# Optimization experiments

Measured on AMD Instinct MI355X. Metric: run time of the kernel, lower is better.

The kernel has to match this reference:

```python
import jax, jax.numpy as jnp
import numpy as np

B_SZ = 8
G = 2048
D_MODEL = 512
D_STATE = 128
D_CONV = 4
EXPAND = 2
HEADDIM = 64
D_INNER = EXPAND * D_MODEL          # 1024
NHEADS = D_INNER // HEADDIM         # 16
CONV_DIM = D_INNER + 2 * D_STATE    # 1280
D_IN_PROJ = 2 * D_INNER + 2 * D_STATE + NHEADS  # 2320
ID_DIM = 128
CHR_DIM = 64
N_CHR = 25
F_LOCUS = 32
PATH_DIM = 128
GENE_FEAT = ID_DIM + PATH_DIM + 2 * CHR_DIM  # 384
N_PERT = 10000
P_DIM = 128


def silu(x):
    return x * jax.nn.sigmoid(x)


def causal_dw_conv(x, w, b):
    # x: (B,L,C), w: (C,K), b: (C,)  causal depthwise conv (left pad K-1)
    K = w.shape[1]
    L = x.shape[1]
    xp = jnp.pad(x, ((0, 0), (K - 1, 0), (0, 0)))
    out = b[None, None, :]
    for k in range(K):
        out = out + xp[:, k:k + L, :] * w[:, k][None, None, :]
    return out


def mamba2(u, in_w, conv_w, conv_b, dt_bias, A_log, Dp, norm_w, out_w):
    # u: (B,L,d_model) -> (B,L,d_model); mamba_ssm Mamba2 defaults, ngroups=1
    Bb, L, _ = u.shape
    zxbcdt = u @ in_w.T                                   # (B,L,D_IN_PROJ)
    z = zxbcdt[..., :D_INNER]
    xBC = zxbcdt[..., D_INNER:D_INNER + CONV_DIM]
    dt = zxbcdt[..., D_INNER + CONV_DIM:]                 # (B,L,H)
    xBC = silu(causal_dw_conv(xBC, conv_w, conv_b))
    x = xBC[..., :D_INNER].reshape(Bb, L, NHEADS, HEADDIM)
    Bm = xBC[..., D_INNER:D_INNER + D_STATE]              # (B,L,N)
    Cm = xBC[..., D_INNER + D_STATE:]                     # (B,L,N)
    dt = jax.nn.softplus(dt + dt_bias)                    # (B,L,H)
    dA = jnp.exp(dt * (-jnp.exp(A_log)))                  # (B,L,H)

    def step(h, inp):
        dA_t, dt_t, B_t, C_t, x_t = inp
        h = dA_t[:, :, None, None] * h + jnp.einsum('bh,bn,bhp->bhpn', dt_t, B_t, x_t)
        y = jnp.einsum('bhpn,bn->bhp', h, C_t)
        return h, y

    h0 = jnp.zeros((Bb, NHEADS, HEADDIM, D_STATE), u.dtype)
    xs = (dA.transpose(1, 0, 2), dt.transpose(1, 0, 2),
          Bm.transpose(1, 0, 2), Cm.transpose(1, 0, 2), x.transpose(1, 0, 2, 3))
    _, ys = jax.lax.scan(step, h0, xs)                    # ys: (L,B,H,P)
    y = ys.transpose(1, 0, 2, 3) + Dp[None, None, :, None] * x
    y = y.reshape(Bb, L, D_INNER)
    # gated RMSNorm (norm_before_gate=False): norm(y * silu(z))
    y = y * silu(z)
    y = y * jax.lax.rsqrt(jnp.mean(y * y, axis=-1, keepdims=True) + 1e-5) * norm_w
    return y @ out_w.T


def setup_inputs() -> dict:
    key = jax.random.key(0)
    ks = iter(jax.random.split(key, 48))

    def nrm(shape, scale):
        return jax.random.normal(next(ks), shape, jnp.float32) * scale

    inp = {}
    inp['perturbation_idx'] = jax.random.randint(next(ks), (B_SZ,), 0, N_PERT)
    inp['chr_idx'] = jax.random.randint(next(ks), (G,), 0, N_CHR)
    inp['locus_fourier'] = nrm((G, 2 * F_LOCUS), 1.0)
    inp['pathway_features'] = nrm((G, PATH_DIM), 1.0)
    inp['pert_emb'] = nrm((N_PERT, P_DIM), 0.02)
    inp['gene_id_emb'] = nrm((G, ID_DIM), 0.02)
    inp['chr_emb'] = nrm((N_CHR, CHR_DIM), 0.02)
    inp['locus_w'] = nrm((CHR_DIM, 2 * F_LOCUS), (2 * F_LOCUS) ** -0.5)
    inp['locus_b'] = jnp.zeros((CHR_DIM,), jnp.float32)
    inp['cond_w'] = nrm((GENE_FEAT, P_DIM), P_DIM ** -0.5)
    inp['cond_b'] = jnp.zeros((GENE_FEAT,), jnp.float32)
    inp['in_w'] = nrm((D_MODEL, GENE_FEAT), GENE_FEAT ** -0.5)
    inp['in_b'] = jnp.zeros((D_MODEL,), jnp.float32)
    inp['head_w'] = nrm((1, D_MODEL), D_MODEL ** -0.5)
    inp['head_b'] = jnp.zeros((1,), jnp.float32)
    for p in ('f_', 'b_'):
        inp[p + 'in_w'] = nrm((D_IN_PROJ, D_MODEL), D_MODEL ** -0.5)
        inp[p + 'conv_w'] = nrm((CONV_DIM, D_CONV), D_CONV ** -0.5)
        inp[p + 'conv_b'] = jnp.zeros((CONV_DIM,), jnp.float32)
        inp[p + 'dt_bias'] = nrm((NHEADS,), 0.5)
        inp[p + 'A_log'] = jnp.log(jax.random.uniform(next(ks), (NHEADS,), jnp.float32, 1.0, 16.0))
        inp[p + 'D'] = jnp.ones((NHEADS,), jnp.float32)
        inp[p + 'norm_w'] = jnp.ones((D_INNER,), jnp.float32)
        inp[p + 'out_w'] = nrm((D_MODEL, D_INNER), D_INNER ** -0.5)
    return inp


def reference(perturbation_idx, chr_idx, locus_fourier, pathway_features,
              pert_emb, gene_id_emb, chr_emb, locus_w, locus_b,
              cond_w, cond_b, in_w, in_b, head_w, head_b,
              f_in_w, f_conv_w, f_conv_b, f_dt_bias, f_A_log, f_D, f_norm_w, f_out_w,
              b_in_w, b_conv_w, b_conv_b, b_dt_bias, b_A_log, b_D, b_norm_w, b_out_w):
    B = perturbation_idx.shape[0]
    cond = pert_emb[perturbation_idx] @ cond_w.T + cond_b          # (B, GENE_FEAT)
    e_chr = chr_emb[chr_idx]                                        # (G, CHR_DIM)
    e_locus = jax.nn.gelu(locus_fourier @ locus_w.T + locus_b, approximate=False)
    gene_feat = jnp.concatenate([gene_id_emb, pathway_features, e_chr, e_locus], axis=1)  # (G, GENE_FEAT)
    seq = jnp.concatenate([cond[:, None, :],
                           jnp.broadcast_to(gene_feat[None], (B,) + gene_feat.shape)], axis=1)
    seq = seq @ in_w.T + in_b                                       # (B, G+1, d_model)
    h_fwd = mamba2(seq, f_in_w, f_conv_w, f_conv_b, f_dt_bias, f_A_log, f_D, f_norm_w, f_out_w)
    h_bwd = jnp.flip(mamba2(jnp.flip(seq, axis=1), b_in_w, b_conv_w, b_conv_b,
                            b_dt_bias, b_A_log, b_D, b_norm_w, b_out_w), axis=1)
    H = h_fwd + h_bwd
    return H[:, 1:, :] @ head_w.T + head_b                          # (B, G, 1)
```

## Files before the change

kernel.cpp:

```cpp
#include <hip/hip_runtime.h>
#include <hip/hip_bf16.h>
#include <hip/hip_fp16.h>
#include <math.h>

#define DPROJ 2320
#define CONVD 1280

typedef __attribute__((ext_vector_type(8))) short bf16x8;
typedef __attribute__((ext_vector_type(4))) float f32x4;

__device__ __forceinline__ float siluf(float x) { return x / (1.f + __expf(-x)); }
__device__ __forceinline__ float bfu(unsigned short s) { return __uint_as_float(((unsigned)s) << 16); }
__device__ __forceinline__ unsigned short f2bf(float f) {
    unsigned u = __float_as_uint(f);
    unsigned r = (u + 0x7FFFu + ((u >> 16) & 1u)) >> 16;
    return (unsigned short)r;
}
__device__ __forceinline__ unsigned short f2h(float f) {
    __half h = __float2half(f);
    return *(unsigned short*)&h;
}
__device__ __forceinline__ float h2f(unsigned short s) {
    __half h = *(__half*)&s;
    return __half2float(h);
}


__global__ void gg_kernel(const int* __restrict__ chridx, const float* __restrict__ gid,
                          const float* __restrict__ path, const float* __restrict__ chrE,
                          const int* __restrict__ pidx, const float* __restrict__ pertE,
                          float* __restrict__ gf, float* __restrict__ cemb,
                          float* __restrict__ wf2, float* __restrict__ wb2) {
    int blk = blockIdx.x, tid = threadIdx.x;
    if (blk < 3072) {
        int idx = blk * 256 + tid;
        int g = idx / 384, j = idx % 384;
        float v;
        if (j < 128)      v = gid[(size_t)g * 128 + j];
        else if (j < 256) v = path[(size_t)g * 128 + (j - 128)];
        else if (j < 320) v = chrE[(size_t)chridx[g] * 64 + (j - 256)];
        else return;
        gf[idx] = v;
    } else if (blk < 3076) {
        int idx = (blk - 3072) * 256 + tid;
        int b = idx >> 7, k = idx & 127;
        cemb[idx] = pertE[(size_t)pidx[b] * 128 + k];
    } else {
        wf2[tid * 4 + 0] = 0.f; wf2[tid * 4 + 1] = 0.f;
        wf2[tid * 4 + 2] = 0.f; wf2[tid * 4 + 3] = 0.f;
        wb2[tid * 4 + 0] = 0.f; wb2[tid * 4 + 1] = 0.f;
        wb2[tid * 4 + 2] = 0.f; wb2[tid * 4 + 3] = 0.f;
    }
}

__global__ void wfold_kernel(const float* __restrict__ headW,
                             const float* __restrict__ fOutW, const float* __restrict__ fNw,
                             const float* __restrict__ bOutW, const float* __restrict__ bNw,
                             float* __restrict__ wf2, float* __restrict__ wb2) {
    int blk = blockIdx.x;
    int dir = blk >> 6;
    int rem = blk & 63;
    int dseg = rem >> 4, mseg = rem & 15;
    int tid = threadIdx.x;
    int d = dseg * 256 + tid;
    const float* W = dir ? bOutW : fOutW;
    float s = 0.f;
#pragma unroll
    for (int m = mseg * 32; m < mseg * 32 + 32; ++m)
        s += headW[m] * W[(size_t)m * 1024 + d];
    const float* nw = dir ? bNw : fNw;
    atomicAdd(&(dir ? wb2 : wf2)[d], s * nw[d]);
}


__global__ void tobf4_kernel(const float* __restrict__ inW, const float* __restrict__ fInW,
                             const float* __restrict__ bInW, const float* __restrict__ gf,
                             unsigned short* __restrict__ inW2, unsigned short* __restrict__ fInW2,
                             unsigned short* __restrict__ bInW2, unsigned short* __restrict__ gf2) {
    size_t idx = (size_t)blockIdx.x * 256 + threadIdx.x;
    const size_t A = 512UL * 384, B5 = 2432UL * 512;
    if (idx < A) {
        inW2[idx] = f2bf(inW[idx]);
    } else if (idx < A + B5) {
        size_t k = idx - A; int m = k / 512, kk = k % 512;
        fInW2[k] = f2bf(m < 2320 ? fInW[(size_t)m * 512 + kk] : 0.f);
    } else if (idx < A + 2 * B5) {
        size_t k = idx - A - B5; int m = k / 512, kk = k % 512;
        bInW2[k] = f2bf(m < 2320 ? bInW[(size_t)m * 512 + kk] : 0.f);
    } else {
        size_t k = idx - A - 2 * B5;
        gf2[k] = f2bf(gf[k]);
    }
}

__global__ void tobf_kernel(const float* __restrict__ in, unsigned short* __restrict__ out,
                            int M, int K, int Mpad) {
    int idx = blockIdx.x * 256 + threadIdx.x;
    if (idx >= Mpad * K) return;
    int m = idx / K, k = idx % K;
    float v = (m < M) ? in[(size_t)m * K + k] : 0.f;
    out[idx] = f2bf(v);
}


__global__ __launch_bounds__(256) void mfma_gemm_kernel(
    const unsigned short* __restrict__ A2, const unsigned short* __restrict__ W2,
    const float* __restrict__ bias, float* __restrict__ C,
    int N, int K2, int ldc) {
    __shared__ __align__(16) unsigned short Al[128 * 40];
    __shared__ __align__(16) unsigned short Bl[128 * 40];
    const int tid = threadIdx.x;
    const int bm = blockIdx.y * 128, bn = blockIdx.x * 128;
    const int lane = tid & 63, wave = tid >> 6;
    const int wm = (wave >> 1) * 64, wn = (wave & 1) * 64;
    f32x4 acc[4][4];
#pragma unroll
    for (int i = 0; i < 4; ++i)
#pragma unroll
        for (int j = 0; j < 4; ++j) acc[i][j] = (f32x4){0.f, 0.f, 0.f, 0.f};

    for (int k0 = 0; k0 < K2; k0 += 32) {
        __syncthreads();
#pragma unroll
        for (int s = 0; s < 2; ++s) {
            int ch = tid + 256 * s;
            int row = ch >> 2, q = ch & 3;
            uint4 va = *(const uint4*)&A2[(size_t)(bm + row) * K2 + k0 + q * 8];
            *(uint4*)&Al[row * 40 + q * 8] = va;
            uint4 vb = *(const uint4*)&W2[(size_t)(bn + row) * K2 + k0 + q * 8];
            *(uint4*)&Bl[row * 40 + q * 8] = vb;
        }
        __syncthreads();
        bf16x8 af[4], bfr[4];
#pragma unroll
        for (int i = 0; i < 4; ++i)
            af[i] = *(const bf16x8*)&Al[(wm + i * 16 + (lane & 15)) * 40 + (lane >> 4) * 8];
#pragma unroll
        for (int j = 0; j < 4; ++j)
            bfr[j] = *(const bf16x8*)&Bl[(wn + j * 16 + (lane & 15)) * 40 + (lane >> 4) * 8];
#pragma unroll
        for (int i = 0; i < 4; ++i)
#pragma unroll
            for (int j = 0; j < 4; ++j)
                acc[i][j] = __builtin_amdgcn_mfma_f32_16x16x32_bf16(af[i], bfr[j], acc[i][j], 0, 0, 0);
    }
#pragma unroll
    for (int i = 0; i < 4; ++i) {
        int m = bm + wm + i * 16 + (lane >> 4) * 4;
#pragma unroll
        for (int j = 0; j < 4; ++j) {
            int n = bn + wn + j * 16 + (lane & 15);
            if (n < N) {
                float bv = bias ? bias[n] : 0.f;
#pragma unroll
                for (int r = 0; r < 4; ++r)
                    C[(size_t)(m + r) * ldc + n] = acc[i][j][r] + bv;
            }
        }
    }
}


__global__ __launch_bounds__(256) void gemm_kernel(
    const float* __restrict__ A, const float* __restrict__ W,
    const float* __restrict__ bias, float* __restrict__ C,
    int M, int N, int K, int ldc, int act) {
    __shared__ __align__(16) float As[16][68];
    __shared__ __align__(16) float Ws[16][68];
    const int tid = threadIdx.x;
    const int tx = tid & 15, ty = tid >> 4;
    const int bm = blockIdx.y * 64, bn = blockIdx.x * 64;
    const int lr = tid >> 2;
    const int lk = (tid & 3) * 4;
    float acc[4][4];
#pragma unroll
    for (int i = 0; i < 4; ++i)
#pragma unroll
        for (int j = 0; j < 4; ++j) acc[i][j] = 0.f;

    for (int k0 = 0; k0 < K; k0 += 16) {
        const int am = bm + lr;
        const int wn = bn + lr;
        float4 av = make_float4(0.f, 0.f, 0.f, 0.f), wv = make_float4(0.f, 0.f, 0.f, 0.f);
        if (am < M) av = *(const float4*)&A[(size_t)am * K + k0 + lk];
        if (wn < N) wv = *(const float4*)&W[(size_t)wn * K + k0 + lk];
        __syncthreads();
        As[lk + 0][lr] = av.x; As[lk + 1][lr] = av.y; As[lk + 2][lr] = av.z; As[lk + 3][lr] = av.w;
        Ws[lk + 0][lr] = wv.x; Ws[lk + 1][lr] = wv.y; Ws[lk + 2][lr] = wv.z; Ws[lk + 3][lr] = wv.w;
        __syncthreads();
#pragma unroll
        for (int kk = 0; kk < 16; ++kk) {
            float4 a = *(const float4*)&As[kk][ty * 4];
            float4 w = *(const float4*)&Ws[kk][tx * 4];
            float aa[4] = {a.x, a.y, a.z, a.w}, ww[4] = {w.x, w.y, w.z, w.w};
#pragma unroll
            for (int i = 0; i < 4; ++i)
#pragma unroll
                for (int j = 0; j < 4; ++j) acc[i][j] += aa[i] * ww[j];
        }
    }
#pragma unroll
    for (int i = 0; i < 4; ++i) {
        const int m = bm + ty * 4 + i;
        if (m >= M) continue;
#pragma unroll
        for (int j = 0; j < 4; ++j) {
            const int n = bn + tx * 4 + j;
            if (n >= N) continue;
            float v = acc[i][j] + (bias ? bias[n] : 0.f);
            if (act == 1) v = 0.5f * v * (1.f + erff(v * 0.70710678118654752f));
            C[(size_t)m * ldc + n] = v;
        }
    }
}


__global__ void elem_kernel(const float* __restrict__ zxf, const float* __restrict__ zxb,
                            const float* __restrict__ zxc,
                            const float* __restrict__ fDtB, const float* __restrict__ bDtB,
                            unsigned short* __restrict__ szF, unsigned short* __restrict__ szB,
                            float* __restrict__ dtFsT, float* __restrict__ dtBsT,
                            float* __restrict__ dtFp) {
    size_t idx = (size_t)blockIdx.x * 256 + threadIdx.x;
    const size_t SZ = 2048UL * 1024;
    if (idx < SZ) {
        size_t j = idx >> 10, d = idx & 1023;
        szF[idx] = f2h(siluf(zxf[j * DPROJ + d]));
    } else if (idx < 2 * SZ) {
        size_t k = idx - SZ;
        size_t j = k >> 10, d = k & 1023;
        szB[k] = f2h(siluf(zxb[j * DPROJ + d]));
    } else if (idx < 2 * SZ + 32768) {
        int k = (int)(idx - 2 * SZ);
        int r = k >> 4, hh = k & 15;
        float raw = zxf[(size_t)r * DPROJ + 2304 + hh] + fDtB[hh];
        dtFsT[hh * 2048 + r] = (raw > 20.f) ? raw : log1pf(expf(raw));
    } else if (idx < 2 * SZ + 65536) {
        int k = (int)(idx - 2 * SZ - 32768);
        int r = k >> 4, hh = k & 15;
        float raw = zxb[(size_t)(2047 - r) * DPROJ + 2304 + hh] + bDtB[hh];
        dtBsT[hh * 2048 + r] = (raw > 20.f) ? raw : log1pf(expf(raw));
    } else if (idx < 2 * SZ + 65536 + 128) {
        int k = (int)(idx - 2 * SZ - 65536);
        int b = k >> 4, hh = k & 15;
        float raw = zxc[(size_t)b * DPROJ + 2304 + hh] + fDtB[hh];
        dtFp[k] = (raw > 20.f) ? raw : log1pf(expf(raw));
    }
}

__global__ void cum_kernel(const float* __restrict__ dtFsT, const float* __restrict__ dtBsT,
                           const float* __restrict__ fAlog, const float* __restrict__ bAlog,
                           float* __restrict__ cumF, float* __restrict__ cumB) {
    int id = blockIdx.x * 256 + threadIdx.x;
    int dir = id >> 9, k = id & 511, h = k >> 5, c = k & 31;
    const float* dtT = dir ? dtBsT : dtFsT;
    const float* Al = dir ? bAlog : fAlog;
    float* cum = dir ? cumB : cumF;
    float a = -expf(Al[h]);
    float acc = 0.f;
    for (int s4 = 0; s4 < 16; ++s4) {
        float4 v = *(const float4*)&dtT[h * 2048 + c * 64 + s4 * 4];
        float4 o;
        acc += v.x * a; o.x = acc;
        acc += v.y * a; o.y = acc;
        acc += v.z * a; o.z = acc;
        acc += v.w * a; o.w = acc;
        *(float4*)&cum[h * 2048 + c * 64 + s4 * 4] = o;
    }
}


__global__ void convFsh_kernel(const float* __restrict__ zxf, const float* __restrict__ cw,
                               const float* __restrict__ cb,
                               unsigned short* __restrict__ bc16, unsigned short* __restrict__ x16) {
    int idx = blockIdx.x * 256 + threadIdx.x;
    if (idx >= 2045 * 1280) return;
    int t4 = idx / 1280, c = idx % 1280;
    float4 w4 = *(const float4*)&cw[c * 4];
    float acc = cb[c];
    acc += zxf[(size_t)(t4 + 0) * DPROJ + 1024 + c] * w4.x;
    acc += zxf[(size_t)(t4 + 1) * DPROJ + 1024 + c] * w4.y;
    acc += zxf[(size_t)(t4 + 2) * DPROJ + 1024 + c] * w4.z;
    acc += zxf[(size_t)(t4 + 3) * DPROJ + 1024 + c] * w4.w;
    float r = siluf(acc);
    if (c >= 1024) bc16[(size_t)t4 * 256 + (c - 1024)] = f2bf(r);
    else           x16[(size_t)t4 * 1024 + c] = f2bf(r);
}

__global__ void convFpb_kernel(const float* __restrict__ zxf, const float* __restrict__ zxc,
                               const float* __restrict__ cw, const float* __restrict__ cb,
                               float* __restrict__ outp, unsigned short* __restrict__ bc16,
                               unsigned short* __restrict__ x16) {
    int idx = blockIdx.x * 256 + threadIdx.x;
    int b = idx / 5120;
    int r = idx % 5120;
    int t = r / 1280, c = r % 1280;
    float4 w4 = *(const float4*)&cw[c * 4];
    float w[4] = {w4.x, w4.y, w4.z, w4.w};
    float acc = cb[c];
#pragma unroll
    for (int k = 0; k < 4; ++k) {
        int j = t - 3 + k;
        float x = 0.f;
        if (j == 0)      x = zxc[(size_t)b * DPROJ + 1024 + c];
        else if (j >= 1) x = zxf[(size_t)(j - 1) * DPROJ + 1024 + c];
        acc += x * w[k];
    }
    float rr = siluf(acc);
    outp[idx] = rr;
    if (c >= 1024) bc16[(size_t)(b * 4 + t) * 256 + (c - 1024)] = f2bf(rr);
    else           x16[(size_t)(b * 4 + t) * 1024 + c] = f2bf(rr);
}

__global__ void convBsh_kernel(const float* __restrict__ zxb, const float* __restrict__ cw,
                               const float* __restrict__ cb,
                               unsigned short* __restrict__ bc16, unsigned short* __restrict__ x16) {
    int idx = blockIdx.x * 256 + threadIdx.x;
    int s = idx / 1280, c = idx % 1280;
    float4 w4 = *(const float4*)&cw[c * 4];
    float w[4] = {w4.x, w4.y, w4.z, w4.w};
    float acc = cb[c];
#pragma unroll
    for (int k = 0; k < 4; ++k) {
        int j = s - 3 + k;
        if (j >= 0) acc += zxb[(size_t)(2047 - j) * DPROJ + 1024 + c] * w[k];
    }
    float r = siluf(acc);
    if (c >= 1024) bc16[(size_t)s * 256 + (c - 1024)] = f2bf(r);
    else           x16[(size_t)s * 1024 + c] = f2bf(r);
}


__global__ __launch_bounds__(256) void intra_kernel(
    const unsigned short* __restrict__ bcF, const unsigned short* __restrict__ bcFp,
    const unsigned short* __restrict__ bcB,
    const unsigned short* __restrict__ xF16, const unsigned short* __restrict__ xFp16,
    const unsigned short* __restrict__ xB16,
    const float* __restrict__ dtFsT, const float* __restrict__ dtBsT,
    const float* __restrict__ cumF, const float* __restrict__ cumB,
    unsigned short* __restrict__ YiF0, unsigned short* __restrict__ YiFs,
    unsigned short* __restrict__ YiB,
    unsigned short* __restrict__ UF0, unsigned short* __restrict__ UFs,
    unsigned short* __restrict__ UB) {
    __shared__ __align__(16) unsigned char smraw[63232];
    unsigned short* Bt = (unsigned short*)smraw;
    unsigned short* Ct = (unsigned short*)(smraw + 17408);
    unsigned short* Sm = (unsigned short*)(smraw + 17408);
    unsigned short* BT = (unsigned short*)(smraw + 34816);
    unsigned short* XT = (unsigned short*)(smraw + 53248);
    float* scum = (float*)(smraw + 62464);
// ... 132 lines not shown

    const int nm = wave * 32;
    f32x4 acc3[2][4];
#pragma unroll
    for (int i = 0; i < 2; ++i)
#pragma unroll
        for (int j = 0; j < 4; ++j) acc3[i][j] = (f32x4){0.f, 0.f, 0.f, 0.f};
#pragma unroll
    for (int ks = 0; ks < 2; ++ks) {
        float ev[8];
#pragma unroll
        for (int jj = 0; jj < 8; ++jj) ev[jj] = se[ks * 32 + quad * 8 + jj];
        bf16x8 bfx[4];
#pragma unroll
        for (int j = 0; j < 4; ++j) {
            bf16x8 xs = *(const bf16x8*)&XT[(j * 16 + l15) * 72 + ks * 32 + quad * 8];
#pragma unroll
            for (int jj = 0; jj < 8; ++jj)
                bfx[j][jj] = (short)f2bf(bfu((unsigned short)xs[jj]) * ev[jj]);
        }
        bf16x8 af[2];
#pragma unroll
        for (int i = 0; i < 2; ++i)
            af[i] = *(const bf16x8*)&BT[(nm + i * 16 + l15) * 72 + ks * 32 + quad * 8];
#pragma unroll
        for (int i = 0; i < 2; ++i)
#pragma unroll
            for (int j = 0; j < 4; ++j)
                acc3[i][j] = __builtin_amdgcn_mfma_f32_16x16x32_bf16(af[i], bfx[j], acc3[i][j], 0, 0, 0);
    }
#pragma unroll
    for (int i = 0; i < 2; ++i)
#pragma unroll
        for (int j = 0; j < 4; ++j) {
            int p = j * 16 + l15;
            int n0 = nm + i * 16 + quad * 4;
            ushort4 o = make_ushort4(f2bf(acc3[i][j][0]), f2bf(acc3[i][j][1]),
                                     f2bf(acc3[i][j][2]), f2bf(acc3[i][j][3]));
            *(ushort4*)&Uout[p * 128 + n0] = o;
        }
}


__global__ void cbm_kernel(const float* __restrict__ convFp, const unsigned short* __restrict__ bcF,
                           const float* __restrict__ dtFp, const float* __restrict__ cumF,
                           const unsigned short* __restrict__ UF0,
                           float* __restrict__ cb0, unsigned short* __restrict__ Mb) {
    int blk = blockIdx.x, tid = threadIdx.x;
    if (blk < 32) {
        int idx = blk * 256 + tid;
        int b = idx >> 10, r = idx & 1023, h = r >> 6, tl = r & 63;
        int t = tl + 1;
        const float* b0 = convFp + (size_t)(b * 4) * CONVD;
        float s = 0.f;
        if (t < 4) {
            const float* crow = convFp + (size_t)(b * 4 + t) * CONVD;
            for (int n = 0; n < 128; ++n) s += crow[1152 + n] * b0[1024 + n];
        } else {
            const unsigned short* cr = bcF + (size_t)(t - 4) * 256 + 128;
            for (int n = 0; n < 128; ++n) s += bfu(cr[n]) * b0[1024 + n];
        }
        cb0[(b * 16 + h) * 64 + tl] = s * dtFp[b * 16 + h];
    } else {
        int bh = blk - 32;
        int b = bh >> 4, h = bh & 15;
        float D0 = __expf(cumF[h * 2048 + 63]);
        float dt0 = dtFp[b * 16 + h];
        const float* row0 = convFp + (size_t)(b * 4) * CONVD;
        const unsigned short* u = UF0 + (size_t)(b * 16 + h) * 8192;
        unsigned short* m = Mb + (size_t)(b * 16 + h) * 8192;
        for (int e4 = tid; e4 < 2048; e4 += 256) {
            int e = e4 * 4, p = e >> 7, n0 = e & 127;
            float s = D0 * dt0 * row0[h * 64 + p];
            float4 B4 = *(const float4*)&row0[1024 + n0];
            ushort4 uv = *(const ushort4*)&u[e];
            ushort4 o = make_ushort4(f2bf(s * B4.x + bfu(uv.x)), f2bf(s * B4.y + bfu(uv.y)),
                                     f2bf(s * B4.z + bfu(uv.z)), f2bf(s * B4.w + bfu(uv.w)));
            *(ushort4*)&m[e] = o;
        }
    }
}


__global__ void tpsi_kernel(const unsigned short* __restrict__ UFs, const unsigned short* __restrict__ UB,
                            const float* __restrict__ cumF, const float* __restrict__ cumB,
                            unsigned short* __restrict__ Tst, float* __restrict__ psiF) {
    int blk = blockIdx.x;
    int dir = blk >> 7, h = (blk >> 3) & 15, q8 = blk & 7;
    int tid = threadIdx.x;
    const unsigned short* U = dir ? UB : UFs;
    const float* cum = dir ? cumB : cumF;
    unsigned short* T = Tst + (size_t)(dir * 16 + h) * 32 * 8192;
    if (dir == 0 && q8 == 0 && tid == 0) {
        float ps = 1.f;
        for (int c = 1; c < 32; ++c) {
            psiF[h * 32 + c] = ps;
            ps *= __expf(cumF[h * 2048 + c * 64 + 63]);
        }
    }
    const size_t e = (size_t)q8 * 1024 + 4 * tid;
    float4 st = make_float4(0.f, 0.f, 0.f, 0.f);
    const int c0 = dir ? 0 : 1;
    ushort4 u = *(const ushort4*)&U[((size_t)c0 * 16 + h) * 8192 + e];
    for (int c = c0; c < 32; ++c) {
        ushort4 un = make_ushort4(0, 0, 0, 0);
        if (c + 1 < 32) un = *(const ushort4*)&U[((size_t)(c + 1) * 16 + h) * 8192 + e];
        float Dc = __expf(cum[h * 2048 + c * 64 + 63]);
        ushort4 o = make_ushort4(f2bf(st.x), f2bf(st.y), f2bf(st.z), f2bf(st.w));
        *(ushort4*)&T[(size_t)c * 8192 + e] = o;
        st.x = Dc * st.x + bfu(u.x);
        st.y = Dc * st.y + bfu(u.y);
        st.z = Dc * st.z + bfu(u.z);
        st.w = Dc * st.w + bfu(u.w);
        u = un;
    }
}


__global__ __launch_bounds__(256) void yt_kernel(
    const unsigned short* __restrict__ bcF, const unsigned short* __restrict__ bcB,
    const unsigned short* __restrict__ Tst,
    unsigned short* __restrict__ YtF, unsigned short* __restrict__ YtB) {
    const int iid = blockIdx.x;
    int dir, h, c;
    if (iid < 496) { dir = 0; c = 1 + (iid >> 4); h = iid & 15; }
    else           { int k = iid - 496; dir = 1; c = k >> 4; h = k & 15; }
    const unsigned short* Cbase = (dir == 0)
        ? bcF + ((size_t)(64 * c - 3)) * 256 + 128
        : bcB + ((size_t)(64 * c)) * 256 + 128;
    const unsigned short* Tp = Tst + ((size_t)(dir * 16 + h) * 32 + c) * 8192;
    unsigned short* Yt = (dir == 0 ? YtF : YtB) + (size_t)(c * 16 + h) * 4096;
    const int tid = threadIdx.x;
    const int lane = tid & 63, wave = tid >> 6;
    const int quad = lane >> 4, l15 = lane & 15;
    const int pm = (wave >> 1) * 32, tb = (wave & 1) * 32;
    f32x4 acc[2][2];
#pragma unroll
    for (int i = 0; i < 2; ++i)
#pragma unroll
        for (int j = 0; j < 2; ++j) acc[i][j] = (f32x4){0.f, 0.f, 0.f, 0.f};
#pragma unroll
    for (int ks = 0; ks < 4; ++ks) {
        bf16x8 af[2], bfr[2];
#pragma unroll
        for (int i = 0; i < 2; ++i)
            af[i] = *(const bf16x8*)&Tp[(size_t)(pm + i * 16 + l15) * 128 + ks * 32 + quad * 8];
#pragma unroll
        for (int j = 0; j < 2; ++j)
            bfr[j] = *(const bf16x8*)&Cbase[(size_t)(tb + j * 16 + l15) * 256 + ks * 32 + quad * 8];
#pragma unroll
        for (int i = 0; i < 2; ++i)
#pragma unroll
            for (int j = 0; j < 2; ++j)
                acc[i][j] = __builtin_amdgcn_mfma_f32_16x16x32_bf16(af[i], bfr[j], acc[i][j], 0, 0, 0);
    }
#pragma unroll
    for (int i = 0; i < 2; ++i)
#pragma unroll
        for (int j = 0; j < 2; ++j) {
            int t = tb + j * 16 + l15;
            int p0 = pm + i * 16 + quad * 4;
            ushort4 o = make_ushort4(f2bf(acc[i][j][0]), f2bf(acc[i][j][1]),
                                     f2bf(acc[i][j][2]), f2bf(acc[i][j][3]));
            *(ushort4*)&Yt[t * 64 + p0] = o;
        }
}


__global__ __launch_bounds__(256) void gate_kernel(
    const unsigned short* __restrict__ bcF,
    const unsigned short* __restrict__ Mb, const float* __restrict__ psiF,
    const unsigned short* __restrict__ YtF, const unsigned short* __restrict__ YtB,
    const unsigned short* __restrict__ xF16, const unsigned short* __restrict__ xFp16,
    const unsigned short* __restrict__ xB16,
    const unsigned short* __restrict__ szF, const unsigned short* __restrict__ szB,
    const float* __restrict__ convFp,
    const float* __restrict__ cumF, const float* __restrict__ cumB,
    const unsigned short* __restrict__ YiF0, const unsigned short* __restrict__ YiFs,
    const unsigned short* __restrict__ YiB,
    const float* __restrict__ cb0,
    const float* __restrict__ fD, const float* __restrict__ bD,
    const float* __restrict__ wf2, const float* __restrict__ wb2,
    float* __restrict__ aF, float* __restrict__ aB) {
    __shared__ __align__(16) float Ysm[64 * 68];

    const int iid = blockIdx.x;
    int dir, b = 0, h, cg;
    if (iid < 1024) { dir = 0; b = iid >> 7; int r = iid & 127; h = r >> 3; cg = r & 7; }
    else            { int k = iid - 1024; dir = 1; h = k >> 3; cg = k & 7; }
    const int tid = threadIdx.x, tx = tid & 15, ty = tid >> 4;
    const int lane = tid & 63, wave = tid >> 6;
    const int quad = lane >> 4, l15 = lane & 15;

    const float Dh = (dir ? bD : fD)[h];
    const float* wvp = dir ? wb2 : wf2;
    float4 wreg = *(const float4*)&wvp[h * 64 + tx * 4];
    const float* cumA = dir ? cumB : cumF;

    const int pm = (wave >> 1) * 32, tb = (wave & 1) * 32;
    bf16x8 mfr[4][2];
    if (dir == 0) {
        const unsigned short* Mp = Mb + (size_t)(b * 16 + h) * 8192;
#pragma unroll
        for (int ks = 0; ks < 4; ++ks)
#pragma unroll
            for (int i = 0; i < 2; ++i)
                mfr[ks][i] = *(const bf16x8*)&Mp[(size_t)(pm + i * 16 + l15) * 128 + ks * 32 + quad * 8];
    }

    for (int cc = 0; cc < 4; ++cc) {
        const int c = cg * 4 + cc;
        const bool fwdG = (dir == 0 && c > 0);
        if (fwdG) {
            if (cc > 0) __syncthreads();
            const unsigned short* Cbase = bcF + ((size_t)(64 * c - 3)) * 256 + 128;
            f32x4 acc[2][2];
#pragma unroll
            for (int i = 0; i < 2; ++i)
#pragma unroll
                for (int j = 0; j < 2; ++j) acc[i][j] = (f32x4){0.f, 0.f, 0.f, 0.f};
#pragma unroll
            for (int ks = 0; ks < 4; ++ks) {
                bf16x8 bfr[2];
#pragma unroll
                for (int j = 0; j < 2; ++j)
                    bfr[j] = *(const bf16x8*)&Cbase[(size_t)(tb + j * 16 + l15) * 256 + ks * 32 + quad * 8];
#pragma unroll
                for (int i = 0; i < 2; ++i)
#pragma unroll
                    for (int j = 0; j < 2; ++j)
                        acc[i][j] = __builtin_amdgcn_mfma_f32_16x16x32_bf16(mfr[ks][i], bfr[j], acc[i][j], 0, 0, 0);
            }
#pragma unroll
            for (int i = 0; i < 2; ++i)
#pragma unroll
                for (int j = 0; j < 2; ++j)
                    *(f32x4*)&Ysm[(tb + j * 16 + l15) * 68 + pm + i * 16 + quad * 4] = acc[i][j];
            __syncthreads();
        }

        const float psi = fwdG ? psiF[h * 32 + c] : 0.f;
        const unsigned short* Ytp = fwdG ? (YtF + (size_t)(c * 16 + h) * 4096)
                                         : (dir ? (YtB + (size_t)(c * 16 + h) * 4096) : nullptr);
        float4 x0v = make_float4(0.f, 0.f, 0.f, 0.f);
        float cbv[4] = {0.f, 0.f, 0.f, 0.f};
        if (dir == 0 && c == 0) {
            x0v = *(const float4*)&convFp[(size_t)(b * 4) * CONVD + h * 64 + tx * 4];
#pragma unroll
// ... 53 lines not shown
            for (int m = 1; m < 16; m <<= 1) {
                a1 += __shfl_xor(a1, m);
                a2 += __shfl_xor(a2, m);
            }
            if (tx == 0) {
                if (dir == 0) {
                    size_t o = ((size_t)(b * 2048 + j) * 16 + h) * 2;
                    aF[o] = a1; aF[o + 1] = a2;
                } else {
                    int g = 2047 - j;
                    size_t o = ((size_t)g * 16 + h) * 2;
                    aB[o] = a1; aB[o + 1] = a2;
                }
            }
        }
    }
}


__global__ void final_kernel(const float* __restrict__ aF, const float* __restrict__ aB,
                             const float* __restrict__ headB, float* __restrict__ out) {
    int idx = blockIdx.x * 256 + threadIdx.x;
    int b = idx >> 11, g = idx & 2047;
    const float* pf = aF + ((size_t)(b * 2048 + g)) * 32;
    const float* pb = aB + (size_t)g * 32;
    float f1 = 0.f, f2 = 0.f, b1 = 0.f, b2 = 0.f;
#pragma unroll
    for (int h = 0; h < 16; ++h) {
        f1 += pf[2 * h]; f2 += pf[2 * h + 1];
        b1 += pb[2 * h]; b2 += pb[2 * h + 1];
    }
    out[idx] = f1 * rsqrtf(f2 * (1.f / 1024.f) + 1e-5f) +
               b1 * rsqrtf(b2 * (1.f / 1024.f) + 1e-5f) + headB[0];
}


extern "C" void kernel_launch(void* const* d_in, const int* in_sizes, int n_in,
                              void* d_out, int out_size, void* d_ws, size_t ws_size,
                              hipStream_t stream) {
    const int*   pidx   = (const int*)  d_in[0];
    const int*   chridx = (const int*)  d_in[1];
    const float* locusF = (const float*)d_in[2];
    const float* pathF  = (const float*)d_in[3];
    const float* pertE  = (const float*)d_in[4];
    const float* gidE   = (const float*)d_in[5];
    const float* chrE   = (const float*)d_in[6];
    const float* locusW = (const float*)d_in[7];
    const float* locusB = (const float*)d_in[8];
    const float* condW  = (const float*)d_in[9];
    const float* condB  = (const float*)d_in[10];
    const float* inW    = (const float*)d_in[11];
    const float* inB    = (const float*)d_in[12];
    const float* headW  = (const float*)d_in[13];
    const float* headB  = (const float*)d_in[14];
    const float* fInW   = (const float*)d_in[15];
    const float* fCw    = (const float*)d_in[16];
    const float* fCb    = (const float*)d_in[17];
    const float* fDtB   = (const float*)d_in[18];
    const float* fAlog  = (const float*)d_in[19];
    const float* fDp    = (const float*)d_in[20];
    const float* fNw    = (const float*)d_in[21];
    const float* fOutW  = (const float*)d_in[22];
    const float* bInW   = (const float*)d_in[23];
    const float* bCw    = (const float*)d_in[24];
    const float* bCb    = (const float*)d_in[25];
    const float* bDtB   = (const float*)d_in[26];
    const float* bAlog  = (const float*)d_in[27];
    const float* bDp    = (const float*)d_in[28];
    const float* bNw    = (const float*)d_in[29];
    const float* bOutW  = (const float*)d_in[30];
    float* out = (float*)d_out;
    (void)in_sizes; (void)n_in; (void)out_size; (void)ws_size;

    char* base = (char*)d_ws;
    size_t off = 0;
    auto allocf = [&](size_t n) -> float* {
        char* r = base + off; off += ((n * 4 + 63) & ~(size_t)63); return (float*)r; };
    auto allocu = [&](size_t n) -> unsigned short* {
        char* r = base + off; off += ((n * 2 + 63) & ~(size_t)63); return (unsigned short*)r; };

    float* gf     = allocf(2048UL * 384);
    float* cond   = allocf(8UL * 384);
    float* cemb   = allocf(8UL * 128);
    float* ug     = allocf(2048UL * 512);
    float* uc     = allocf(8UL * 512);
    float* zxf    = allocf(2048UL * DPROJ);
    float* zxb    = allocf(2048UL * DPROJ);
    float* zxc    = allocf(8UL * DPROJ);
    float* convFp = allocf(8UL * 4 * CONVD);
    float* dtFsT  = allocf(16UL * 2048);
    float* dtFp   = allocf(128);
    float* dtBsT  = allocf(16UL * 2048);
    float* cumF   = allocf(16UL * 2048);
    float* cumB   = allocf(16UL * 2048);
    float* wf2    = allocf(1024);
    float* wb2    = allocf(1024);
    float* cb0    = allocf(8UL * 16 * 64);
    float* psiF   = allocf(16UL * 32);
    float* aF     = allocf(8UL * 2048 * 16 * 2);
    float* aB     = allocf(2048UL * 16 * 2);
    unsigned short* YiF0 = allocu(8UL * 16 * 4096);
    unsigned short* YiFs = allocu(32UL * 16 * 4096);
    unsigned short* YiB  = allocu(32UL * 16 * 4096);
    unsigned short* UF0  = allocu(8UL * 16 * 8192);
    unsigned short* UFs  = allocu(32UL * 16 * 8192);
    unsigned short* UB   = allocu(32UL * 16 * 8192);
    unsigned short* Mb   = allocu(8UL * 16 * 8192);
    unsigned short* Tst  = allocu(2UL * 16 * 32 * 8192);
    unsigned short* bcF  = allocu(2045UL * 256);
    unsigned short* bcFp = allocu(32UL * 256);
    unsigned short* bcB  = allocu(2048UL * 256);
    unsigned short* YtF  = allocu(32UL * 16 * 4096);
    unsigned short* YtB  = allocu(32UL * 16 * 4096);
    unsigned short* xF16 = allocu(2045UL * 1024);
    unsigned short* xFp16= allocu(32UL * 1024);
    unsigned short* xB16 = allocu(2048UL * 1024);
    unsigned short* szF  = allocu(2048UL * 1024);
    unsigned short* szB  = allocu(2048UL * 1024);
    unsigned short* gf2   = allocu(2048UL * 384);
    unsigned short* inW2  = allocu(512UL * 384);
    unsigned short* ug2   = allocu(2048UL * 512);
    unsigned short* fInW2 = allocu(2432UL * 512);
    unsigned short* bInW2 = allocu(2432UL * 512);

    gg_kernel<<<3077, 256, 0, stream>>>(chridx, gidE, pathF, chrE, pidx, pertE, gf, cemb, wf2, wb2);
    wfold_kernel<<<128, 256, 0, stream>>>(headW, fOutW, fNw, bOutW, bNw, wf2, wb2);
    gemm_kernel<<<dim3(1, 32), 256, 0, stream>>>(locusF, locusW, locusB, gf + 320, 2048, 64, 64, 384, 1);
    gemm_kernel<<<dim3(6, 1), 256, 0, stream>>>(cemb, condW, condB, cond, 8, 384, 128, 384, 0);

    tobf4_kernel<<<13568, 256, 0, stream>>>(inW, fInW, bInW, gf, inW2, fInW2, bInW2, gf2);

    mfma_gemm_kernel<<<dim3(4, 16), 256, 0, stream>>>(gf2, inW2, inB, ug, 512, 384, 512);
    gemm_kernel<<<dim3(8, 1), 256, 0, stream>>>(cond, inW, inB, uc, 8, 512, 384, 512, 0);

    tobf_kernel<<<(2048 * 512 + 255) / 256, 256, 0, stream>>>(ug, ug2, 2048, 512, 2048);
    mfma_gemm_kernel<<<dim3(19, 16), 256, 0, stream>>>(ug2, fInW2, nullptr, zxf, 2320, 512, 2320);
    mfma_gemm_kernel<<<dim3(19, 16), 256, 0, stream>>>(ug2, bInW2, nullptr, zxb, 2320, 512, 2320);
    gemm_kernel<<<dim3(37, 1), 256, 0, stream>>>(uc, fInW, nullptr, zxc, 8, DPROJ, 512, DPROJ, 0);

    elem_kernel<<<16641, 256, 0, stream>>>(zxf, zxb, zxc, fDtB, bDtB, szF, szB, dtFsT, dtBsT, dtFp);
    cum_kernel<<<4, 256, 0, stream>>>(dtFsT, dtBsT, fAlog, bAlog, cumF, cumB);
    convFsh_kernel<<<(2045 * 1280 + 255) / 256, 256, 0, stream>>>(zxf, fCw, fCb, bcF, xF16);
    convFpb_kernel<<<160, 256, 0, stream>>>(zxf, zxc, fCw, fCb, convFp, bcFp, xFp16);
    convBsh_kernel<<<10240, 256, 0, stream>>>(zxb, bCw, bCb, bcB, xB16);
    intra_kernel<<<1136, 256, 0, stream>>>(bcF, bcFp, bcB, xF16, xFp16, xB16,
                                           dtFsT, dtBsT, cumF, cumB,
                                           YiF0, YiFs, YiB, UF0, UFs, UB);
    cbm_kernel<<<160, 256, 0, stream>>>(convFp, bcF, dtFp, cumF, UF0, cb0, Mb);
    tpsi_kernel<<<256, 256, 0, stream>>>(UFs, UB, cumF, cumB, Tst, psiF);
    yt_kernel<<<1008, 256, 0, stream>>>(bcF, bcB, Tst, YtF, YtB);
    gate_kernel<<<1152, 256, 0, stream>>>(bcF, Mb, psiF, YtF, YtB, xF16, xFp16, xB16,
                                          szF, szB, convFp, cumF, cumB,
                                          YiF0, YiFs, YiB, cb0, fDp, bDp, wf2, wb2, aF, aB);
    final_kernel<<<64, 256, 0, stream>>>(aF, aB, headB, out);
}
```

Baseline: 398.4 us.

## Fuse bf16/silu epilogues into GEMMs, softplus into cumsum, and state scan with Yt

The input GEMM now writes bf16 output directly, which removes the separate fp32 buffer and the tobf conversion kernel. The zxbcdt GEMMs apply silu(z) in their epilogue and store it as fp16. The dt softplus moves into the cumulative-sum kernel, which removes elem_kernel. The chunk-state recurrence and the Yt MFMA product now run in one kernel that keeps each state in LDS, so the Tst global round trip is gone. The catch is that this fused kernel launches only 32 blocks and walks the 32 chunks serially, where before two kernels with many more blocks did this work in parallel.

```diff
diff --git a/kernel.cpp b/kernel.cpp
--- a/kernel.cpp
+++ b/kernel.cpp
@@ -93,19 +93,11 @@
     }
 }
 
-__global__ void tobf_kernel(const float* __restrict__ in, unsigned short* __restrict__ out,
-                            int M, int K, int Mpad) {
-    int idx = blockIdx.x * 256 + threadIdx.x;
-    if (idx >= Mpad * K) return;
-    int m = idx / K, k = idx % K;
-    float v = (m < M) ? in[(size_t)m * K + k] : 0.f;
-    out[idx] = f2bf(v);
-}
-
 
 __global__ __launch_bounds__(256) void mfma_gemm_kernel(
     const unsigned short* __restrict__ A2, const unsigned short* __restrict__ W2,
     const float* __restrict__ bias, float* __restrict__ C,
+    unsigned short* __restrict__ Cbf, unsigned short* __restrict__ sz,
     int N, int K2, int ldc) {
     __shared__ __align__(16) unsigned short Al[128 * 40];
     __shared__ __align__(16) unsigned short Bl[128 * 40];
@@ -153,8 +145,15 @@
             if (n < N) {
                 float bv = bias ? bias[n] : 0.f;
 #pragma unroll
-                for (int r = 0; r < 4; ++r)
-                    C[(size_t)(m + r) * ldc + n] = acc[i][j][r] + bv;
+                for (int r = 0; r < 4; ++r) {
+                    float v = acc[i][j][r] + bv;
+                    if (sz && n < 1024)
+                        sz[(size_t)(m + r) * 1024 + n] = f2h(siluf(v));
+                    else if (Cbf)
+                        Cbf[(size_t)(m + r) * ldc + n] = f2bf(v);
+                    else
+                        C[(size_t)(m + r) * ldc + n] = v;
+                }
             }
         }
     }
@@ -215,57 +214,38 @@
 }
 
 
-__global__ void elem_kernel(const float* __restrict__ zxf, const float* __restrict__ zxb,
-                            const float* __restrict__ zxc,
-                            const float* __restrict__ fDtB, const float* __restrict__ bDtB,
-                            unsigned short* __restrict__ szF, unsigned short* __restrict__ szB,
-                            float* __restrict__ dtFsT, float* __restrict__ dtBsT,
-                            float* __restrict__ dtFp) {
-    size_t idx = (size_t)blockIdx.x * 256 + threadIdx.x;
-    const size_t SZ = 2048UL * 1024;
-    if (idx < SZ) {
-        size_t j = idx >> 10, d = idx & 1023;
-        szF[idx] = f2h(siluf(zxf[j * DPROJ + d]));
-    } else if (idx < 2 * SZ) {
-        size_t k = idx - SZ;
-        size_t j = k >> 10, d = k & 1023;
-        szB[k] = f2h(siluf(zxb[j * DPROJ + d]));
-    } else if (idx < 2 * SZ + 32768) {
-        int k = (int)(idx - 2 * SZ);
-        int r = k >> 4, hh = k & 15;
-        float raw = zxf[(size_t)r * DPROJ + 2304 + hh] + fDtB[hh];
-        dtFsT[hh * 2048 + r] = (raw > 20.f) ? raw : log1pf(expf(raw));
-    } else if (idx < 2 * SZ + 65536) {
-        int k = (int)(idx - 2 * SZ - 32768);
-        int r = k >> 4, hh = k & 15;
-        float raw = zxb[(size_t)(2047 - r) * DPROJ + 2304 + hh] + bDtB[hh];
-        dtBsT[hh * 2048 + r] = (raw > 20.f) ? raw : log1pf(expf(raw));
-    } else if (idx < 2 * SZ + 65536 + 128) {
-        int k = (int)(idx - 2 * SZ - 65536);
-        int b = k >> 4, hh = k & 15;
-        float raw = zxc[(size_t)b * DPROJ + 2304 + hh] + fDtB[hh];
-        dtFp[k] = (raw > 20.f) ? raw : log1pf(expf(raw));
-    }
-}
-
-__global__ void cum_kernel(const float* __restrict__ dtFsT, const float* __restrict__ dtBsT,
+__global__ void cum_kernel(const float* __restrict__ zxf, const float* __restrict__ zxb,
+                           const float* __restrict__ zxc,
+                           const float* __restrict__ fDtB, const float* __restrict__ bDtB,
                            const float* __restrict__ fAlog, const float* __restrict__ bAlog,
+                           float* __restrict__ dtFsT, float* __restrict__ dtBsT,
+                           float* __restrict__ dtFp,
                            float* __restrict__ cumF, float* __restrict__ cumB) {
-    int id = blockIdx.x * 256 + threadIdx.x;
+    int blk = blockIdx.x, tid = threadIdx.x;
+    if (blk == 4) {
+        if (tid < 128) {
+            int b = tid >> 4, h = tid & 15;
+            float raw = zxc[(size_t)b * DPROJ + 2304 + h] + fDtB[h];
+            dtFp[tid] = (raw > 20.f) ? raw : log1pf(expf(raw));
+        }
+        return;
+    }
+    int id = blk * 256 + tid;
     int dir = id >> 9, k = id & 511, h = k >> 5, c = k & 31;
-    const float* dtT = dir ? dtBsT : dtFsT;
-    const float* Al = dir ? bAlog : fAlog;
+    const float* zx = dir ? zxb : zxf;
+    float bias = (dir ? bDtB : fDtB)[h];
+    float a = -expf((dir ? bAlog : fAlog)[h]);
+    float* dtT = dir ? dtBsT : dtFsT;
     float* cum = dir ? cumB : cumF;
-    float a = -expf(Al[h]);
     float acc = 0.f;
-    for (int s4 = 0; s4 < 16; ++s4) {
-        float4 v = *(const float4*)&dtT[h * 2048 + c * 64 + s4 * 4];
-        float4 o;
-        acc += v.x * a; o.x = acc;
-        acc += v.y * a; o.y = acc;
-        acc += v.z * a; o.z = acc;
-        acc += v.w * a; o.w = acc;
-        *(float4*)&cum[h * 2048 + c * 64 + s4 * 4] = o;
+    for (int s = 0; s < 64; ++s) {
+        int j = c * 64 + s;
+        int row = dir ? (2047 - j) : j;
+        float raw = zx[(size_t)row * DPROJ + 2304 + h] + bias;
+        float dt = (raw > 20.f) ? raw : log1pf(expf(raw));
+        dtT[h * 2048 + j] = dt;
+        acc += dt * a;
+        cum[h * 2048 + j] = acc;
     }
 }
 
@@ -564,88 +544,100 @@
 }
 
 
-__global__ void tpsi_kernel(const unsigned short* __restrict__ UFs, const unsigned short* __restrict__ UB,
-                            const float* __restrict__ cumF, const float* __restrict__ cumB,
-                            unsigned short* __restrict__ Tst, float* __restrict__ psiF) {
-    int blk = blockIdx.x;
-    int dir = blk >> 7, h = (blk >> 3) & 15, q8 = blk & 7;
-    int tid = threadIdx.x;
+__global__ __launch_bounds__(256) void tyt_kernel(
+    const unsigned short* __restrict__ UFs, const unsigned short* __restrict__ UB,
+    const unsigned short* __restrict__ bcF, const unsigned short* __restrict__ bcB,
+    const float* __restrict__ cumF, const float* __restrict__ cumB,
+    unsigned short* __restrict__ YtF, unsigned short* __restrict__ YtB,
+    float* __restrict__ psiF) {
+    __shared__ __align__(16) unsigned short Tl[64 * 136];
+    const int blk = blockIdx.x;
+    const int dir = blk >> 4, h = blk & 15;
     const unsigned short* U = dir ? UB : UFs;
     const float* cum = dir ? cumB : cumF;
-    unsigned short* T = Tst + (size_t)(dir * 16 + h) * 32 * 8192;
-    if (dir == 0 && q8 == 0 && tid == 0) {
+    unsigned short* Yt = dir ? YtB : YtF;
+    const int tid = threadIdx.x;
+    const int lane = tid & 63, wave = tid >> 6;
+    const int quad = lane >> 4, l15 = lane & 15;
+    const int pm = (wave >> 1) * 32, tb = (wave & 1) * 32;
+
+    if (dir == 0 && tid == 0) {
         float ps = 1.f;
         for (int c = 1; c < 32; ++c) {
             psiF[h * 32 + c] = ps;
             ps *= __expf(cumF[h * 2048 + c * 64 + 63]);
         }
     }
-    const size_t e = (size_t)q8 * 1024 + 4 * tid;
-    float4 st = make_float4(0.f, 0.f, 0.f, 0.f);
+
+    f32x4 st[8];
+#pragma unroll
+    for (int q = 0; q < 8; ++q) st[q] = (f32x4){0.f, 0.f, 0.f, 0.f};
     const int c0 = dir ? 0 : 1;
-    ushort4 u = *(const ushort4*)&U[((size_t)c0 * 16 + h) * 8192 + e];
+    ushort4 u[8];
+#pragma unroll
+    for (int q = 0; q < 8; ++q)
+        u[q] = *(const ushort4*)&U[((size_t)c0 * 16 + h) * 8192 + q * 1024 + 4 * tid];
+
     for (int c = c0; c < 32; ++c) {
-        ushort4 un = make_ushort4(0, 0, 0, 0);
-        if (c + 1 < 32) un = *(const ushort4*)&U[((size_t)(c + 1) * 16 + h) * 8192 + e];
+#pragma unroll
+        for (int q = 0; q < 8; ++q) {
+            int e = q * 1024 + 4 * tid;
+            int p = e >> 7, n = e & 127;
+            ushort4 o = make_ushort4(f2bf(st[q][0]), f2bf(st[q][1]), f2bf(st[q][2]), f2bf(st[q][3]));
+            *(ushort4*)&Tl[p * 136 + n] = o;
+        }
+        __syncthreads();
+        ushort4 un[8];
+#pragma unroll
+        for (int q = 0; q < 8; ++q) un[q] = make_ushort4(0, 0, 0, 0);
+        if (c + 1 < 32)
+#pragma unroll
+            for (int q = 0; q < 8; ++q)
+                un[q] = *(const ushort4*)&U[((size_t)(c + 1) * 16 + h) * 8192 + q * 1024 + 4 * tid];
+        const unsigned short* Cbase = dir ? bcB + ((size_t)(64 * c)) * 256 + 128
+                                          : bcF + ((size_t)(64 * c - 3)) * 256 + 128;
+        f32x4 acc[2][2];
+#pragma unroll
+        for (int i = 0; i < 2; ++i)
+#pragma unroll
+            for (int j = 0; j < 2; ++j) acc[i][j] = (f32x4){0.f, 0.f, 0.f, 0.f};
+#pragma unroll
+        for (int ks = 0; ks < 4; ++ks) {
+            bf16x8 af[2], bfr[2];
+#pragma unroll
+            for (int i = 0; i < 2; ++i)
+                af[i] = *(const bf16x8*)&Tl[(pm + i * 16 + l15) * 136 + ks * 32 + quad * 8];
+#pragma unroll
+            for (int j = 0; j < 2; ++j)
+                bfr[j] = *(const bf16x8*)&Cbase[(size_t)(tb + j * 16 + l15) * 256 + ks * 32 + quad * 8];
+#pragma unroll
+            for (int i = 0; i < 2; ++i)
+#pragma unroll
+                for (int j = 0; j < 2; ++j)
+                    acc[i][j] = __builtin_amdgcn_mfma_f32_16x16x32_bf16(af[i], bfr[j], acc[i][j], 0, 0, 0);
+        }
+        unsigned short* Yc = Yt + (size_t)(c * 16 + h) * 4096;
+#pragma unroll
+        for (int i = 0; i < 2; ++i)
+#pragma unroll
+            for (int j = 0; j < 2; ++j) {
+                int t = tb + j * 16 + l15;
+                int p0 = pm + i * 16 + quad * 4;
+                ushort4 o = make_ushort4(f2bf(acc[i][j][0]), f2bf(acc[i][j][1]),
+                                         f2bf(acc[i][j][2]), f2bf(acc[i][j][3]));
+                *(ushort4*)&Yc[t * 64 + p0] = o;
+            }
         float Dc = __expf(cum[h * 2048 + c * 64 + 63]);
-        ushort4 o = make_ushort4(f2bf(st.x), f2bf(st.y), f2bf(st.z), f2bf(st.w));
-        *(ushort4*)&T[(size_t)c * 8192 + e] = o;
-        st.x = Dc * st.x + bfu(u.x);
-        st.y = Dc * st.y + bfu(u.y);
-        st.z = Dc * st.z + bfu(u.z);
-        st.w = Dc * st.w + bfu(u.w);
-        u = un;
-    }
-}
-
-
-__global__ __launch_bounds__(256) void yt_kernel(
-    const unsigned short* __restrict__ bcF, const unsigned short* __restrict__ bcB,
-    const unsigned short* __restrict__ Tst,
-    unsigned short* __restrict__ YtF, unsigned short* __restrict__ YtB) {
-    const int iid = blockIdx.x;
-    int dir, h, c;
-    if (iid < 496) { dir = 0; c = 1 + (iid >> 4); h = iid & 15; }
-    else           { int k = iid - 496; dir = 1; c = k >> 4; h = k & 15; }
-    const unsigned short* Cbase = (dir == 0)
-        ? bcF + ((size_t)(64 * c - 3)) * 256 + 128
-        : bcB + ((size_t)(64 * c)) * 256 + 128;
-    const unsigned short* Tp = Tst + ((size_t)(dir * 16 + h) * 32 + c) * 8192;
-    unsigned short* Yt = (dir == 0 ? YtF : YtB) + (size_t)(c * 16 + h) * 4096;
-    const int tid = threadIdx.x;
-    const int lane = tid & 63, wave = tid >> 6;
-    const int quad = lane >> 4, l15 = lane & 15;
-    const int pm = (wave >> 1) * 32, tb = (wave & 1) * 32;
-    f32x4 acc[2][2];
-#pragma unroll
-    for (int i = 0; i < 2; ++i)
-#pragma unroll
-        for (int j = 0; j < 2; ++j) acc[i][j] = (f32x4){0.f, 0.f, 0.f, 0.f};
-#pragma unroll
-    for (int ks = 0; ks < 4; ++ks) {
-        bf16x8 af[2], bfr[2];
-#pragma unroll
-        for (int i = 0; i < 2; ++i)
-            af[i] = *(const bf16x8*)&Tp[(size_t)(pm + i * 16 + l15) * 128 + ks * 32 + quad * 8];
-#pragma unroll
-        for (int j = 0; j < 2; ++j)
-            bfr[j] = *(const bf16x8*)&Cbase[(size_t)(tb + j * 16 + l15) * 256 + ks * 32 + quad * 8];
-#pragma unroll
-        for (int i = 0; i < 2; ++i)
-#pragma unroll
-            for (int j = 0; j < 2; ++j)
-                acc[i][j] = __builtin_amdgcn_mfma_f32_16x16x32_bf16(af[i], bfr[j], acc[i][j], 0, 0, 0);
-    }
-#pragma unroll
-    for (int i = 0; i < 2; ++i)
-#pragma unroll
-        for (int j = 0; j < 2; ++j) {
-            int t = tb + j * 16 + l15;
-            int p0 = pm + i * 16 + quad * 4;
-            ushort4 o = make_ushort4(f2bf(acc[i][j][0]), f2bf(acc[i][j][1]),
-                                     f2bf(acc[i][j][2]), f2bf(acc[i][j][3]));
-            *(ushort4*)&Yt[t * 64 + p0] = o;
-        }
+#pragma unroll
+        for (int q = 0; q < 8; ++q) {
+            st[q][0] = Dc * st[q][0] + bfu(u[q].x);
+            st[q][1] = Dc * st[q][1] + bfu(u[q].y);
+            st[q][2] = Dc * st[q][2] + bfu(u[q].z);
+            st[q][3] = Dc * st[q][3] + bfu(u[q].w);
+            u[q] = un[q];
+        }
+        __syncthreads();
+    }
 }
 
 
@@ -865,7 +857,6 @@
     float* gf     = allocf(2048UL * 384);
     float* cond   = allocf(8UL * 384);
     float* cemb   = allocf(8UL * 128);
-    float* ug     = allocf(2048UL * 512);
     float* uc     = allocf(8UL * 512);
     float* zxf    = allocf(2048UL * DPROJ);
     float* zxb    = allocf(2048UL * DPROJ);
@@ -889,7 +880,6 @@
     unsigned short* UFs  = allocu(32UL * 16 * 8192);
     unsigned short* UB   = allocu(32UL * 16 * 8192);
     unsigned short* Mb   = allocu(8UL * 16 * 8192);
-    unsigned short* Tst  = allocu(2UL * 16 * 32 * 8192);
     unsigned short* bcF  = allocu(2045UL * 256);
     unsigned short* bcFp = allocu(32UL * 256);
     unsigned short* bcB  = allocu(2048UL * 256);
@@ -913,16 +903,15 @@
 
     tobf4_kernel<<<13568, 256, 0, stream>>>(inW, fInW, bInW, gf, inW2, fInW2, bInW2, gf2);
 
-    mfma_gemm_kernel<<<dim3(4, 16), 256, 0, stream>>>(gf2, inW2, inB, ug, 512, 384, 512);
+    mfma_gemm_kernel<<<dim3(4, 16), 256, 0, stream>>>(gf2, inW2, inB, nullptr, ug2, nullptr, 512, 384, 512);
     gemm_kernel<<<dim3(8, 1), 256, 0, stream>>>(cond, inW, inB, uc, 8, 512, 384, 512, 0);
 
-    tobf_kernel<<<(2048 * 512 + 255) / 256, 256, 0, stream>>>(ug, ug2, 2048, 512, 2048);
-    mfma_gemm_kernel<<<dim3(19, 16), 256, 0, stream>>>(ug2, fInW2, nullptr, zxf, 2320, 512, 2320);
-    mfma_gemm_kernel<<<dim3(19, 16), 256, 0, stream>>>(ug2, bInW2, nullptr, zxb, 2320, 512, 2320);
+    mfma_gemm_kernel<<<dim3(19, 16), 256, 0, stream>>>(ug2, fInW2, nullptr, zxf, nullptr, szF, 2320, 512, DPROJ);
+    mfma_gemm_kernel<<<dim3(19, 16), 256, 0, stream>>>(ug2, bInW2, nullptr, zxb, nullptr, szB, 2320, 512, DPROJ);
     gemm_kernel<<<dim3(37, 1), 256, 0, stream>>>(uc, fInW, nullptr, zxc, 8, DPROJ, 512, DPROJ, 0);
 
-    elem_kernel<<<16641, 256, 0, stream>>>(zxf, zxb, zxc, fDtB, bDtB, szF, szB, dtFsT, dtBsT, dtFp);
-    cum_kernel<<<4, 256, 0, stream>>>(dtFsT, dtBsT, fAlog, bAlog, cumF, cumB);
+    cum_kernel<<<5, 256, 0, stream>>>(zxf, zxb, zxc, fDtB, bDtB, fAlog, bAlog,
+                                      dtFsT, dtBsT, dtFp, cumF, cumB);
     convFsh_kernel<<<(2045 * 1280 + 255) / 256, 256, 0, stream>>>(zxf, fCw, fCb, bcF, xF16);
     convFpb_kernel<<<160, 256, 0, stream>>>(zxf, zxc, fCw, fCb, convFp, bcFp, xFp16);
     convBsh_kernel<<<10240, 256, 0, stream>>>(zxb, bCw, bCb, bcB, xB16);
@@ -930,8 +919,7 @@
                                            dtFsT, dtBsT, cumF, cumB,
                                            YiF0, YiFs, YiB, UF0, UFs, UB);
     cbm_kernel<<<160, 256, 0, stream>>>(convFp, bcF, dtFp, cumF, UF0, cb0, Mb);
-    tpsi_kernel<<<256, 256, 0, stream>>>(UFs, UB, cumF, cumB, Tst, psiF);
-    yt_kernel<<<1008, 256, 0, stream>>>(bcF, bcB, Tst, YtF, YtB);
+    tyt_kernel<<<32, 256, 0, stream>>>(UFs, UB, bcF, bcB, cumF, cumB, YtF, YtB, psiF);
     gate_kernel<<<1152, 256, 0, stream>>>(bcF, Mb, psiF, YtF, YtB, xF16, xFp16, xB16,
                                           szF, szB, convFp, cumF, cumB,
                                           YiF0, YiFs, YiB, cb0, fDp, bDp, wf2, wb2, aF, aB);
```

Measured after the change: 478.1 us. +20.0%, slower.
